# Optimization experiments

Measured on AMD Instinct MI355X. Metric: run time of the kernel, lower is better.

## Reference

```python
import jax, jax.numpy as jnp
import numpy as np

D_MODEL = 1024
NUM_HEADS = 16
HEAD_DIM = D_MODEL // NUM_HEADS  # 64
# NOTE: the torch module passes scale=attention_head_size (NOT 1/sqrt(dh));
# we reproduce that exact math: scores are MULTIPLIED by head_dim.
SCALE = float(HEAD_DIM)

B, S = 2, 2048


def setup_inputs() -> dict:
    key = jax.random.key(0)
    ks = jax.random.split(key, 6)
    q = jax.random.normal(ks[0], (B, S, D_MODEL), dtype=jnp.float32)
    k = jax.random.normal(ks[1], (B, S, D_MODEL), dtype=jnp.float32)
    v = jax.random.normal(ks[2], (B, S, D_MODEL), dtype=jnp.float32)
    # Linear weights stored as [in, out]; scaled like typical init so the
    # (head_dim-scaled) logits stay numerically sane.
    w_std = 0.02
    Wq = jax.random.normal(ks[3], (D_MODEL, D_MODEL), dtype=jnp.float32) * w_std
    Wk = jax.random.normal(ks[4], (D_MODEL, D_MODEL), dtype=jnp.float32) * w_std
    Wv = jax.random.normal(ks[5], (D_MODEL, D_MODEL), dtype=jnp.float32) * w_std
    return {"q": q, "k": k, "v": v, "Wq": Wq, "Wk": Wk, "Wv": Wv}


def reference(q, k, v, Wq, Wk, Wv):
    Bq, Sq, _ = q.shape
    # QKV projections (qkv_bias=False), split into heads: [B, S, H, dh]
    qh = (q @ Wq).reshape(Bq, Sq, NUM_HEADS, HEAD_DIM)
    kh = (k @ Wk).reshape(Bq, Sq, NUM_HEADS, HEAD_DIM)
    vh = (v @ Wv).reshape(Bq, Sq, NUM_HEADS, HEAD_DIM)
    # Full materialized scores [B, H, Sq, Sk] -- the naive MHA pattern.
    sims = jnp.einsum("bqhd,bkhd->bhqk", qh, kh) * SCALE
    attn = jax.nn.softmax(sims, axis=-1)
    # Second matmul, then merge heads back: [B, S, D]
    out = jnp.einsum("bhqk,bkhd->bqhd", attn, vh).reshape(Bq, Sq, D_MODEL)
    return out
```

## Files before the change

kernel.cpp:

```cpp
#include <hip/hip_runtime.h>
#include <cstdint>
#include <cstddef>

typedef unsigned short u16;
typedef __bf16 bf16x8 __attribute__((ext_vector_type(8)));
typedef float f32x4 __attribute__((ext_vector_type(4)));
typedef unsigned int u32x4 __attribute__((ext_vector_type(4)));
typedef unsigned int u32x2 __attribute__((ext_vector_type(2)));
typedef u16 u16x4 __attribute__((ext_vector_type(4)));

typedef __attribute__((address_space(3))) void lds_void;
typedef __attribute__((address_space(1))) void glb_void;

constexpr float CEXP = 92.33248261689366f;

constexpr size_t XSZ = 4096ull * 1024ull;
constexpr size_t WSZ = 1024ull * 1024ull;
constexpr size_t OFF_XQH = 0;
constexpr size_t OFF_XQL = OFF_XQH + XSZ;
constexpr size_t OFF_XKH = OFF_XQL + XSZ;
constexpr size_t OFF_XKL = OFF_XKH + XSZ;
constexpr size_t OFF_XVH = OFF_XKL + XSZ;
constexpr size_t OFF_XVL = OFF_XVH + XSZ;
constexpr size_t OFF_WQH = OFF_XVL + XSZ;
constexpr size_t OFF_WQL = OFF_WQH + WSZ;
constexpr size_t OFF_WKH = OFF_WQL + WSZ;
constexpr size_t OFF_WKL = OFF_WKH + WSZ;
constexpr size_t OFF_WVH = OFF_WKL + WSZ;
constexpr size_t OFF_WVL = OFF_WVH + WSZ;
constexpr size_t OFF_QH  = OFF_WVL + WSZ;
constexpr size_t OFF_QL  = OFF_QH + XSZ;
constexpr size_t OFF_KH  = OFF_QL + XSZ;
constexpr size_t OFF_KL  = OFF_KH + XSZ;
constexpr size_t OFF_VH  = OFF_KL + XSZ;
constexpr size_t OFF_VT  = OFF_VH + XSZ;

__device__ __forceinline__ u16 f2b(float f) {
  unsigned u = __builtin_bit_cast(unsigned, f);
  return (u16)((u + 0x7FFFu + ((u >> 16) & 1u)) >> 16);
}
__device__ __forceinline__ float b2f(u16 h) {
  return __builtin_bit_cast(float, ((unsigned)h) << 16);
}
__device__ __forceinline__ bf16x8 ld8(const u16* p) {
  return __builtin_bit_cast(bf16x8, *(const u32x4*)p);
}
__device__ __forceinline__ unsigned pk2(float a, float b) {
#if __has_builtin(__builtin_amdgcn_cvt_pk_bf16_f32)
  auto v = __builtin_amdgcn_cvt_pk_bf16_f32(a, b);
  return __builtin_bit_cast(unsigned, v);
#else
  return (unsigned)f2b(a) | ((unsigned)f2b(b) << 16);
#endif
}
__device__ __forceinline__ float ex2(float x) {
#if __has_builtin(__builtin_amdgcn_exp2f)
  return __builtin_amdgcn_exp2f(x);
#else
  return exp2f(x);
#endif
}
__device__ __forceinline__ void glds16(const u16* g, u16* l) {
  __builtin_amdgcn_global_load_lds((const glb_void*)g, (lds_void*)l, 16, 0, 0);
}
__device__ __forceinline__ int swz32(int row, int cg) {
  return row * 32 + ((cg ^ ((row >> 1) & 3)) * 8);
}
__device__ __forceinline__ int swz64(int row, int cg) {
  return row * 64 + ((cg ^ (row & 7)) * 8);
}

__global__ __launch_bounds__(256) void convert_all(const float* __restrict__ q,
                                                   const float* __restrict__ k,
                                                   const float* __restrict__ v,
                                                   const float* __restrict__ Wq,
                                                   const float* __restrict__ Wk,
                                                   const float* __restrict__ Wv,
                                                   u16* __restrict__ ws) {
  __shared__ float tile[32][33];
  int id = blockIdx.x;
  int t = threadIdx.x;
  if (id < 12288) {
    int z = id >> 12, blk = id & 4095;
    const float* in = (z == 0) ? q : (z == 1) ? k : v;
    u16* hi = ws + ((z == 0) ? OFF_XQH : (z == 1) ? OFF_XKH : OFF_XVH);
    u16* lo = ws + ((z == 0) ? OFF_XQL : (z == 1) ? OFF_XKL : OFF_XVL);
    size_t i = ((size_t)blk * 256u + t) * 4u;
    float4 vv = *(const float4*)(in + i);
    float a[4] = {vv.x, vv.y, vv.z, vv.w};
    u16x4 hv, lv;
#pragma unroll
    for (int j = 0; j < 4; ++j) {
      u16 hb = f2b(a[j]);
      hv[j] = hb;
      lv[j] = f2b(a[j] - b2f(hb));
    }
    *(u16x4*)(hi + i) = hv;
    if (z != 2) *(u16x4*)(lo + i) = lv;
  } else {
    int r0 = id - 12288;
    int z = r0 >> 10, rem = r0 & 1023;
    const float* W = (z == 0) ? Wq : (z == 1) ? Wk : Wv;
    u16* hiT = ws + ((z == 0) ? OFF_WQH : (z == 1) ? OFF_WKH : OFF_WVH);
    u16* loT = ws + ((z == 0) ? OFF_WQL : (z == 1) ? OFF_WKL : OFF_WVL);
    int n0 = (rem & 31) * 32, k0 = (rem >> 5) * 32;
    int r = t >> 3, c0 = (t & 7) * 4;
    float4 vv = *(const float4*)(W + (size_t)(k0 + r) * 1024 + n0 + c0);
    tile[r][c0] = vv.x; tile[r][c0 + 1] = vv.y; tile[r][c0 + 2] = vv.z; tile[r][c0 + 3] = vv.w;
    __syncthreads();
    u16x4 hv, lv;
#pragma unroll
    for (int j = 0; j < 4; ++j) {
      float x = tile[c0 + j][r];
      u16 hb = f2b(x);
      hv[j] = hb;
      lv[j] = f2b(x - b2f(hb));
    }
    size_t o = (size_t)(n0 + r) * 1024 + k0 + c0;
    *(u16x4*)(hiT + o) = hv;
    if (z != 2) *(u16x4*)(loT + o) = lv;
  }
}

__global__ __launch_bounds__(256, 4) void gemm_qkv(u16* __restrict__ ws) {
  __shared__ u16 sA[2][64 * 32];
  __shared__ u16 sB[2][128 * 32];
  u16* cbuf = &sB[0][0];

  int id = blockIdx.x;
  int xcd = id & 7, seq = id >> 3;
  int pair = (seq >> 3) * 8 + xcd;
  int tile_n = seq & 7;
  int z = pair >> 6;
  int tile_m = pair & 63;

  const u16 *Ah, *Al, *Bh, *Bl; u16 *Oh, *Ol; bool split;
  if (z == 0)      { Ah = ws + OFF_XQH; Al = ws + OFF_XQL; Bh = ws + OFF_WQH; Bl = ws + OFF_WQL; Oh = ws + OFF_QH; Ol = ws + OFF_QL; split = true; }
  else if (z == 1) { Ah = ws + OFF_XKH; Al = ws + OFF_XKL; Bh = ws + OFF_WKH; Bl = ws + OFF_WKL; Oh = ws + OFF_KH; Ol = ws + OFF_KL; split = true; }
  else             { Ah = ws + OFF_XVH; Al = nullptr;      Bh = ws + OFF_WVH; Bl = nullptr;      Oh = ws + OFF_VT; Ol = nullptr;    split = false; }
  float oscale = (z == 0) ? CEXP : 1.0f;
  int m0 = tile_m * 64, n0 = tile_n * 128;
  int t = threadIdx.x, lane = t & 63, wave = t >> 6;
  int quad = lane >> 4, l15 = lane & 15;
  int wm = (wave >> 1) * 32, wn = (wave & 1) * 64;
  int rl = lane >> 2, cgl = lane & 3;
  f32x4 acc[2][4] = {};

  int rowA = wave * 16 + rl;
  size_t gA = (size_t)(m0 + rowA) * 1024 + (cgl ^ ((rowA >> 1) & 3)) * 8;
  int lbA = wave * 512;
  size_t gB[2]; int lbB[2];
#pragma unroll
  for (int i = 0; i < 2; ++i) {
    int rowB = wave * 32 + i * 16 + rl;
    gB[i] = (size_t)(n0 + rowB) * 1024 + (cgl ^ ((rowB >> 1) & 3)) * 8;
    lbB[i] = wave * 1024 + i * 512;
  }

  for (int kb = 0; kb < 32; ++kb) {
    int k0 = kb * 32;
    __syncthreads();
    glds16(Ah + gA + k0, &sA[0][lbA]);
    if (split) glds16(Al + gA + k0, &sA[1][lbA]);
#pragma unroll
    for (int i = 0; i < 2; ++i) {
      glds16(Bh + gB[i] + k0, &sB[0][lbB[i]]);
      if (split) glds16(Bl + gB[i] + k0, &sB[1][lbB[i]]);
    }
    __syncthreads();
    bf16x8 afh[2], afl[2], bfh[4], bfl[4];
#pragma unroll
    for (int mt = 0; mt < 2; ++mt) {
      int ra = wm + mt * 16 + l15;
      afh[mt] = ld8(&sA[0][swz32(ra, quad)]);
      if (split) afl[mt] = ld8(&sA[1][swz32(ra, quad)]);
    }
#pragma unroll
    for (int nt = 0; nt < 4; ++nt) {
      int rb = wn + nt * 16 + l15;
      bfh[nt] = ld8(&sB[0][swz32(rb, quad)]);
      if (split) bfl[nt] = ld8(&sB[1][swz32(rb, quad)]);
    }
#pragma unroll
    for (int mt = 0; mt < 2; ++mt)
#pragma unroll
      for (int nt = 0; nt < 4; ++nt) {
        acc[mt][nt] = __builtin_amdgcn_mfma_f32_16x16x32_bf16(afh[mt], bfh[nt], acc[mt][nt], 0, 0, 0);
        if (split) {
          acc[mt][nt] = __builtin_amdgcn_mfma_f32_16x16x32_bf16(afl[mt], bfh[nt], acc[mt][nt], 0, 0, 0);
          acc[mt][nt] = __builtin_amdgcn_mfma_f32_16x16x32_bf16(afh[mt], bfl[nt], acc[mt][nt], 0, 0, 0);
        }
      }
  }
  auto epi_round = [&](u16* dst, bool lo_round) {
#pragma unroll
    for (int mt = 0; mt < 2; ++mt)
#pragma unroll
      for (int nt = 0; nt < 4; ++nt)
#pragma unroll
        for (int r = 0; r < 4; ++r) {
          int row = wm + mt * 16 + quad * 4 + r;
          int col = wn + nt * 16 + l15;
          float v = acc[mt][nt][r] * oscale;
          u16 hb = f2b(v);
          u16 val = lo_round ? f2b(v - b2f(hb)) : hb;
          cbuf[row * 128 + (((col >> 3) ^ (row & 15)) * 8) + (col & 7)] = val;
        }
    __syncthreads();
    int row = t >> 2, seg = t & 3;
    int gm = m0 + row, bb = gm >> 11, s = gm & 2047;
    int hh = (n0 >> 6) + (seg >> 1), d0 = (seg & 1) * 32;
    u16* gp = dst + ((size_t)(bb * 16 + hh) * 2048 + s) * 64 + d0;
#pragma unroll
    for (int i = 0; i < 4; ++i) {
      int phys = (seg * 4 + i) ^ (row & 15);
      *(u32x4*)(gp + i * 8) = *(const u32x4*)(&cbuf[row * 128 + phys * 8]);
    }
  };
  __syncthreads();
  if (split) {
    epi_round(Oh, false);
    __syncthreads();
    epi_round(Ol, true);
  } else {
#pragma unroll
    for (int mt = 0; mt < 2; ++mt)
#pragma unroll
      for (int nt = 0; nt < 4; ++nt)
#pragma unroll
        for (int r = 0; r < 4; ++r) {
          int row = wm + mt * 16 + quad * 4 + r;
          int col = wn + nt * 16 + l15;
          cbuf[row * 128 + (((col >> 3) ^ (row & 15)) * 8) + (col & 7)] =
              f2b(acc[mt][nt][r]);
        }
    __syncthreads();
    int col = t >> 1, sh = t & 1;
    int hg = (n0 + col) >> 6, d = (n0 + col) & 63;
    int bb = m0 >> 11, s0 = m0 & 2047;
    u16 vals[32];
#pragma unroll
    for (int i = 0; i < 32; ++i) {
      int row = sh * 32 + i;
      vals[i] = cbuf[row * 128 + (((col >> 3) ^ (row & 15)) * 8) + (col & 7)];
    }
    u16* gp = Oh + ((size_t)((bb * 16 + hg) * 64 + d)) * 2048 + s0 + sh * 32;
#pragma unroll
    for (int i = 0; i < 4; ++i)
      *(u32x4*)(gp + i * 8) = *(const u32x4*)(&vals[i * 8]);
  }
}

__global__ __launch_bounds__(256, 4) void attn(const u16* __restrict__ ws,
                                               float* __restrict__ out) {
  __shared__ u16 lkh[64 * 64];
  __shared__ u16 lkl[64 * 64];
  __shared__ u16 lvt[64 * 64];
  __shared__ u16 lp[4][16 * 64];
  const u16* Qh = ws + OFF_QH; const u16* Ql = ws + OFF_QL;
  const u16* Kh = ws + OFF_KH; const u16* Kl = ws + OFF_KL;
  const u16* Vt = ws + OFF_VT;
  int id = blockIdx.x;
  int xcd = id & 7, slot = id >> 3;
  int hh = xcd * 4 + (slot >> 5);
  int q0 = (slot & 31) * 64;
  int b = hh >> 4, h = hh & 15;
  int t = threadIdx.x, lane = t & 63, wave = t >> 6;
  int quad = lane >> 4, l15 = lane & 15;
  size_t hb = (size_t)hh * (2048 * 64);
  bf16x8 onesf;
#pragma unroll
  for (int j = 0; j < 8; ++j) onesf[j] = __builtin_bit_cast(__bf16, (u16)0x3F80);
  int qrow = q0 + wave * 16 + l15;
  bf16x8 qfh[2], qfl[2];
#pragma unroll
  for (int ks = 0; ks < 2; ++ks) {
    size_t qo = hb + (size_t)qrow * 64 + ks * 32 + quad * 8;
    qfh[ks] = ld8(Qh + qo);
    qfl[ks] = ld8(Ql + qo);
  }
  float mi = -1e30f;
  f32x4 lsum = {};
  f32x4 o[4] = {};
  int rl = lane >> 3, cgl = lane & 7;

  size_t aK[2], aV[2]; int lb[2];
#pragma unroll
  for (int i = 0; i < 2; ++i) {
    int row = wave * 16 + i * 8 + rl;
    int cgg = cgl ^ (row & 7);
    aK[i] = hb + (size_t)row * 64 + cgg * 8;
    aV[i] = hb + (size_t)row * 2048 + cgg * 8;
    lb[i] = (wave * 16 + i * 8) * 64;
  }
  int soF[2][4];
#pragma unroll
  for (int ks = 0; ks < 2; ++ks)
#pragma unroll
    for (int nt = 0; nt < 4; ++nt)
      soF[ks][nt] = swz64(nt * 16 + l15, ks * 4 + quad);
  int soP[4];
  {
    int r7 = l15 & 7;
#pragma unroll
    for (int nt = 0; nt < 4; ++nt) {
      int c = nt * 2 + (quad >> 1);
      soP[nt] = l15 * 64 + ((c ^ r7) * 8) + (quad & 1) * 4;
    }
  }
  int soPa[2];
#pragma unroll
  for (int ks = 0; ks < 2; ++ks) soPa[ks] = swz64(l15, ks * 4 + quad);
  u16* lpw = &lp[wave][0];

#pragma unroll
  for (int i = 0; i < 2; ++i) {
    glds16(Kh + aK[i], &lkh[lb[i]]);
    glds16(Kl + aK[i], &lkl[lb[i]]);
    glds16(Vt + aV[i], &lvt[lb[i]]);
  }
  __syncthreads();

  for (int kt = 0; kt < 32; ++kt) {
    u32x4 pk_[2], pl_[2], pv_[2];
    if (kt < 31) {
#pragma unroll
      for (int i = 0; i < 2; ++i) {
        pk_[i] = *(const u32x4*)(Kh + aK[i] + (kt + 1) * 4096);
        pl_[i] = *(const u32x4*)(Kl + aK[i] + (kt + 1) * 4096);
        pv_[i] = *(const u32x4*)(Vt + aV[i] + (kt + 1) * 64);
      }
    }
    f32x4 sc[4] = {};
    __builtin_amdgcn_s_setprio(1);
#pragma unroll
    for (int nt = 0; nt < 4; ++nt) {
#pragma unroll
      for (int ks = 0; ks < 2; ++ks) {
        bf16x8 kh_ = ld8(&lkh[soF[ks][nt]]);
        bf16x8 kl_ = ld8(&lkl[soF[ks][nt]]);
        sc[nt] = __builtin_amdgcn_mfma_f32_16x16x32_bf16(kh_, qfh[ks], sc[nt], 0, 0, 0);
        sc[nt] = __builtin_amdgcn_mfma_f32_16x16x32_bf16(kl_, qfh[ks], sc[nt], 0, 0, 0);
        sc[nt] = __builtin_amdgcn_mfma_f32_16x16x32_bf16(kh_, qfl[ks], sc[nt], 0, 0, 0);
      }
    }
    __builtin_amdgcn_s_setprio(0);
    float t0 = fmaxf(fmaxf(sc[0][0], sc[0][1]), sc[0][2]);
    float t1 = fmaxf(fmaxf(sc[0][3], sc[1][0]), sc[1][1]);
    float t2 = fmaxf(fmaxf(sc[1][2], sc[1][3]), sc[2][0]);
    float t3 = fmaxf(fmaxf(sc[2][1], sc[2][2]), sc[2][3]);
    float t4 = fmaxf(fmaxf(sc[3][0], sc[3][1]), sc[3][2]);
    float mx = fmaxf(fmaxf(fmaxf(t0, t1), fmaxf(t2, t3)), fmaxf(t4, sc[3][3]));
    mx = fmaxf(mx, __shfl_xor(mx, 16));
    mx = fmaxf(mx, __shfl_xor(mx, 32));
    float mi_old = mi;
    float mn = fmaxf(mi, mx);
    unsigned long long grew = __ballot(mx > mi);
    mi = mn;
#pragma unroll
    for (int nt = 0; nt < 4; ++nt) {
      unsigned u01 = pk2(ex2(sc[nt][0] - mn), ex2(sc[nt][1] - mn));
      unsigned u23 = pk2(ex2(sc[nt][2] - mn), ex2(sc[nt][3] - mn));
      *(u32x2*)(&lpw[soP[nt]]) = u32x2{u01, u23};
    }
    if (grew) {
      float alpha_s = ex2(mi_old - mn);
      float av[4];
#pragma unroll
      for (int r = 0; r < 4; ++r) av[r] = __shfl(alpha_s, quad * 4 + r);
#pragma unroll
      for (int r = 0; r < 4; ++r) {
        lsum[r] *= av[r];
        o[0][r] *= av[r]; o[1][r] *= av[r]; o[2][r] *= av[r]; o[3][r] *= av[r];
      }
    }
    asm volatile("s_waitcnt lgkmcnt(0)" ::: "memory");
    bf16x8 pa[2];
#pragma unroll
    for (int ks = 0; ks < 2; ++ks) pa[ks] = ld8(&lpw[soPa[ks]]);
    __builtin_amdgcn_s_setprio(1);
    lsum = __builtin_amdgcn_mfma_f32_16x16x32_bf16(pa[0], onesf, lsum, 0, 0, 0);
    lsum = __builtin_amdgcn_mfma_f32_16x16x32_bf16(pa[1], onesf, lsum, 0, 0, 0);
#pragma unroll
    for (int nt = 0; nt < 4; ++nt)
#pragma unroll
      for (int ks = 0; ks < 2; ++ks) {
        bf16x8 bv = ld8(&lvt[soF[ks][nt]]);
        o[nt] = __builtin_amdgcn_mfma_f32_16x16x32_bf16(pa[ks], bv, o[nt], 0, 0, 0);
      }
    __builtin_amdgcn_s_setprio(0);
    __syncthreads();
    if (kt < 31) {
#pragma unroll
      for (int i = 0; i < 2; ++i) {
        *(u32x4*)(&lkh[lb[i] + lane * 8]) = pk_[i];
        *(u32x4*)(&lkl[lb[i] + lane * 8]) = pl_[i];
        *(u32x4*)(&lvt[lb[i] + lane * 8]) = pv_[i];
      }
    }
    __syncthreads();
  }
  float inv[4];
#pragma unroll
  for (int r = 0; r < 4; ++r) inv[r] = 1.0f / lsum[r];
#pragma unroll
  for (int nt = 0; nt < 4; ++nt)
#pragma unroll
    for (int r = 0; r < 4; ++r) {
      int srow = q0 + wave * 16 + quad * 4 + r;
      int d = nt * 16 + l15;
      out[(size_t)(b * 2048 + srow) * 1024 + h * 64 + d] = o[nt][r] * inv[r];
    }
}

extern "C" void kernel_launch(void* const* d_in, const int* in_sizes, int n_in,
                              void* d_out, int out_size, void* d_ws, size_t ws_size,
                              hipStream_t stream) {
  const float* q  = (const float*)d_in[0];
  const float* k  = (const float*)d_in[1];
  const float* v  = (const float*)d_in[2];
  const float* Wq = (const float*)d_in[3];
  const float* Wk = (const float*)d_in[4];
  const float* Wv = (const float*)d_in[5];
  u16* ws = (u16*)d_ws;
  float* out = (float*)d_out;

  convert_all<<<15360, 256, 0, stream>>>(q, k, v, Wq, Wk, Wv, ws);
  gemm_qkv<<<1536, 256, 0, stream>>>(ws);
  attn<<<1024, 256, 0, stream>>>(ws, out);
}
```

Baseline: 270.7 us.

## Process two 16-row query groups per wave and skip negligible score tiles

Each wave now handles 32 query rows as two groups, so every K/V tile loaded into LDS is reused for twice as many queries. The block count halves and the occupancy hint drops to 2. It also skips the exponentiation and PV MFMAs for a group when the tile's max falls far below the running max, treating those probabilities as zero. This trades extra registers and lower occupancy for fewer global loads and less work, and the skip introduces a small approximation.

```diff
diff --git a/kernel.cpp b/kernel.cpp
--- a/kernel.cpp
+++ b/kernel.cpp
@@ -251,19 +251,19 @@
   }
 }
 
-__global__ __launch_bounds__(256, 4) void attn(const u16* __restrict__ ws,
+__global__ __launch_bounds__(256, 2) void attn(const u16* __restrict__ ws,
                                                float* __restrict__ out) {
   __shared__ u16 lkh[64 * 64];
   __shared__ u16 lkl[64 * 64];
   __shared__ u16 lvt[64 * 64];
-  __shared__ u16 lp[4][16 * 64];
+  __shared__ u16 lp[4][2][16 * 64];
   const u16* Qh = ws + OFF_QH; const u16* Ql = ws + OFF_QL;
   const u16* Kh = ws + OFF_KH; const u16* Kl = ws + OFF_KL;
   const u16* Vt = ws + OFF_VT;
   int id = blockIdx.x;
   int xcd = id & 7, slot = id >> 3;
-  int hh = xcd * 4 + (slot >> 5);
-  int q0 = (slot & 31) * 64;
+  int hh = xcd * 4 + (slot >> 4);
+  int q0 = (slot & 15) * 128;
   int b = hh >> 4, h = hh & 15;
   int t = threadIdx.x, lane = t & 63, wave = t >> 6;
   int quad = lane >> 4, l15 = lane & 15;
@@ -271,17 +271,20 @@
   bf16x8 onesf;
 #pragma unroll
   for (int j = 0; j < 8; ++j) onesf[j] = __builtin_bit_cast(__bf16, (u16)0x3F80);
-  int qrow = q0 + wave * 16 + l15;
-  bf16x8 qfh[2], qfl[2];
-#pragma unroll
-  for (int ks = 0; ks < 2; ++ks) {
-    size_t qo = hb + (size_t)qrow * 64 + ks * 32 + quad * 8;
-    qfh[ks] = ld8(Qh + qo);
-    qfl[ks] = ld8(Ql + qo);
-  }
-  float mi = -1e30f;
-  f32x4 lsum = {};
-  f32x4 o[4] = {};
+  bf16x8 qfh[2][2], qfl[2][2];
+#pragma unroll
+  for (int g = 0; g < 2; ++g) {
+    int qrow = q0 + wave * 32 + g * 16 + l15;
+#pragma unroll
+    for (int ks = 0; ks < 2; ++ks) {
+      size_t qo = hb + (size_t)qrow * 64 + ks * 32 + quad * 8;
+      qfh[g][ks] = ld8(Qh + qo);
+      qfl[g][ks] = ld8(Ql + qo);
+    }
+  }
+  float mi[2] = {-1e30f, -1e30f};
+  f32x4 lsum[2] = {};
+  f32x4 o[2][4] = {};
   int rl = lane >> 3, cgl = lane & 7;
 
   size_t aK[2], aV[2]; int lb[2];
@@ -311,7 +314,7 @@
   int soPa[2];
 #pragma unroll
   for (int ks = 0; ks < 2; ++ks) soPa[ks] = swz64(l15, ks * 4 + quad);
-  u16* lpw = &lp[wave][0];
+  u16* lpw[2] = {&lp[wave][0][0], &lp[wave][1][0]};
 
 #pragma unroll
   for (int i = 0; i < 2; ++i) {
@@ -331,7 +334,7 @@
         pv_[i] = *(const u32x4*)(Vt + aV[i] + (kt + 1) * 64);
       }
     }
-    f32x4 sc[4] = {};
+    f32x4 sc[2][4] = {};
     __builtin_amdgcn_s_setprio(1);
 #pragma unroll
     for (int nt = 0; nt < 4; ++nt) {
@@ -339,56 +342,83 @@
       for (int ks = 0; ks < 2; ++ks) {
         bf16x8 kh_ = ld8(&lkh[soF[ks][nt]]);
         bf16x8 kl_ = ld8(&lkl[soF[ks][nt]]);
-        sc[nt] = __builtin_amdgcn_mfma_f32_16x16x32_bf16(kh_, qfh[ks], sc[nt], 0, 0, 0);
-        sc[nt] = __builtin_amdgcn_mfma_f32_16x16x32_bf16(kl_, qfh[ks], sc[nt], 0, 0, 0);
-        sc[nt] = __builtin_amdgcn_mfma_f32_16x16x32_bf16(kh_, qfl[ks], sc[nt], 0, 0, 0);
+#pragma unroll
+        for (int g = 0; g < 2; ++g) {
+          sc[g][nt] = __builtin_amdgcn_mfma_f32_16x16x32_bf16(kh_, qfh[g][ks], sc[g][nt], 0, 0, 0);
+          sc[g][nt] = __builtin_amdgcn_mfma_f32_16x16x32_bf16(kl_, qfh[g][ks], sc[g][nt], 0, 0, 0);
+          sc[g][nt] = __builtin_amdgcn_mfma_f32_16x16x32_bf16(kh_, qfl[g][ks], sc[g][nt], 0, 0, 0);
+        }
       }
     }
     __builtin_amdgcn_s_setprio(0);
-    float t0 = fmaxf(fmaxf(sc[0][0], sc[0][1]), sc[0][2]);
-    float t1 = fmaxf(fmaxf(sc[0][3], sc[1][0]), sc[1][1]);
-    float t2 = fmaxf(fmaxf(sc[1][2], sc[1][3]), sc[2][0]);
-    float t3 = fmaxf(fmaxf(sc[2][1], sc[2][2]), sc[2][3]);
-    float t4 = fmaxf(fmaxf(sc[3][0], sc[3][1]), sc[3][2]);
-    float mx = fmaxf(fmaxf(fmaxf(t0, t1), fmaxf(t2, t3)), fmaxf(t4, sc[3][3]));
-    mx = fmaxf(mx, __shfl_xor(mx, 16));
-    mx = fmaxf(mx, __shfl_xor(mx, 32));
-    float mi_old = mi;
-    float mn = fmaxf(mi, mx);
-    unsigned long long grew = __ballot(mx > mi);
-    mi = mn;
-#pragma unroll
-    for (int nt = 0; nt < 4; ++nt) {
-      unsigned u01 = pk2(ex2(sc[nt][0] - mn), ex2(sc[nt][1] - mn));
-      unsigned u23 = pk2(ex2(sc[nt][2] - mn), ex2(sc[nt][3] - mn));
-      *(u32x2*)(&lpw[soP[nt]]) = u32x2{u01, u23};
-    }
-    if (grew) {
-      float alpha_s = ex2(mi_old - mn);
-      float av[4];
-#pragma unroll
-      for (int r = 0; r < 4; ++r) av[r] = __shfl(alpha_s, quad * 4 + r);
-#pragma unroll
-      for (int r = 0; r < 4; ++r) {
-        lsum[r] *= av[r];
-        o[0][r] *= av[r]; o[1][r] *= av[r]; o[2][r] *= av[r]; o[3][r] *= av[r];
-      }
-    }
-    asm volatile("s_waitcnt lgkmcnt(0)" ::: "memory");
-    bf16x8 pa[2];
-#pragma unroll
-    for (int ks = 0; ks < 2; ++ks) pa[ks] = ld8(&lpw[soPa[ks]]);
-    __builtin_amdgcn_s_setprio(1);
-    lsum = __builtin_amdgcn_mfma_f32_16x16x32_bf16(pa[0], onesf, lsum, 0, 0, 0);
-    lsum = __builtin_amdgcn_mfma_f32_16x16x32_bf16(pa[1], onesf, lsum, 0, 0, 0);
-#pragma unroll
-    for (int nt = 0; nt < 4; ++nt)
-#pragma unroll
-      for (int ks = 0; ks < 2; ++ks) {
-        bf16x8 bv = ld8(&lvt[soF[ks][nt]]);
-        o[nt] = __builtin_amdgcn_mfma_f32_16x16x32_bf16(pa[ks], bv, o[nt], 0, 0, 0);
-      }
-    __builtin_amdgcn_s_setprio(0);
+    bool live[2], grew[2];
+    float mn[2];
+#pragma unroll
+    for (int g = 0; g < 2; ++g) {
+      float t0 = fmaxf(fmaxf(sc[g][0][0], sc[g][0][1]), sc[g][0][2]);
+      float t1 = fmaxf(fmaxf(sc[g][0][3], sc[g][1][0]), sc[g][1][1]);
+      float t2 = fmaxf(fmaxf(sc[g][1][2], sc[g][1][3]), sc[g][2][0]);
+      float t3 = fmaxf(fmaxf(sc[g][2][1], sc[g][2][2]), sc[g][2][3]);
+      float t4 = fmaxf(fmaxf(sc[g][3][0], sc[g][3][1]), sc[g][3][2]);
+      float mx = fmaxf(fmaxf(fmaxf(t0, t1), fmaxf(t2, t3)), fmaxf(t4, sc[g][3][3]));
+      mx = fmaxf(mx, __shfl_xor(mx, 16));
+      mx = fmaxf(mx, __shfl_xor(mx, 32));
+      float mo = mi[g];
+      live[g] = __ballot(mx > mo - 28.0f) != 0ull;
+      grew[g] = __ballot(mx > mo) != 0ull;
+      mn[g] = fmaxf(mo, mx);
+    }
+#pragma unroll
+    for (int g = 0; g < 2; ++g) {
+      if (live[g]) {
+        float m = mn[g];
+#pragma unroll
+        for (int nt = 0; nt < 4; ++nt) {
+          unsigned u01 = pk2(ex2(sc[g][nt][0] - m), ex2(sc[g][nt][1] - m));
+          unsigned u23 = pk2(ex2(sc[g][nt][2] - m), ex2(sc[g][nt][3] - m));
+          *(u32x2*)(&lpw[g][soP[nt]]) = u32x2{u01, u23};
+        }
+        if (grew[g]) {
+          float alpha_s = ex2(mi[g] - m);
+          float av[4];
+#pragma unroll
+          for (int r = 0; r < 4; ++r) av[r] = __shfl(alpha_s, quad * 4 + r);
+#pragma unroll
+          for (int r = 0; r < 4; ++r) {
+            lsum[g][r] *= av[r];
+            o[g][0][r] *= av[r]; o[g][1][r] *= av[r];
+            o[g][2][r] *= av[r]; o[g][3][r] *= av[r];
+          }
+        }
+        mi[g] = m;
+      }
+    }
+    if (live[0] | live[1]) {
+      asm volatile("s_waitcnt lgkmcnt(0)" ::: "memory");
+      bf16x8 pa[2][2];
+#pragma unroll
+      for (int g = 0; g < 2; ++g)
+        if (live[g]) {
+#pragma unroll
+          for (int ks = 0; ks < 2; ++ks) pa[g][ks] = ld8(&lpw[g][soPa[ks]]);
+        }
+      __builtin_amdgcn_s_setprio(1);
+#pragma unroll
+      for (int g = 0; g < 2; ++g)
+        if (live[g]) {
+          lsum[g] = __builtin_amdgcn_mfma_f32_16x16x32_bf16(pa[g][0], onesf, lsum[g], 0, 0, 0);
+          lsum[g] = __builtin_amdgcn_mfma_f32_16x16x32_bf16(pa[g][1], onesf, lsum[g], 0, 0, 0);
+        }
+#pragma unroll
+      for (int nt = 0; nt < 4; ++nt)
+#pragma unroll
+        for (int ks = 0; ks < 2; ++ks) {
+          bf16x8 bv = ld8(&lvt[soF[ks][nt]]);
+          if (live[0]) o[0][nt] = __builtin_amdgcn_mfma_f32_16x16x32_bf16(pa[0][ks], bv, o[0][nt], 0, 0, 0);
+          if (live[1]) o[1][nt] = __builtin_amdgcn_mfma_f32_16x16x32_bf16(pa[1][ks], bv, o[1][nt], 0, 0, 0);
+        }
+      __builtin_amdgcn_s_setprio(0);
+    }
     __syncthreads();
     if (kt < 31) {
 #pragma unroll
@@ -400,17 +430,20 @@
     }
     __syncthreads();
   }
-  float inv[4];
-#pragma unroll
-  for (int r = 0; r < 4; ++r) inv[r] = 1.0f / lsum[r];
-#pragma unroll
-  for (int nt = 0; nt < 4; ++nt)
-#pragma unroll
-    for (int r = 0; r < 4; ++r) {
-      int srow = q0 + wave * 16 + quad * 4 + r;
-      int d = nt * 16 + l15;
-      out[(size_t)(b * 2048 + srow) * 1024 + h * 64 + d] = o[nt][r] * inv[r];
-    }
+#pragma unroll
+  for (int g = 0; g < 2; ++g) {
+    float inv[4];
+#pragma unroll
+    for (int r = 0; r < 4; ++r) inv[r] = 1.0f / lsum[g][r];
+#pragma unroll
+    for (int nt = 0; nt < 4; ++nt)
+#pragma unroll
+      for (int r = 0; r < 4; ++r) {
+        int srow = q0 + wave * 32 + g * 16 + quad * 4 + r;
+        int d = nt * 16 + l15;
+        out[(size_t)(b * 2048 + srow) * 1024 + h * 64 + d] = o[g][nt][r] * inv[r];
+      }
+  }
 }
 
 extern "C" void kernel_launch(void* const* d_in, const int* in_sizes, int n_in,
@@ -427,5 +460,5 @@
 
   convert_all<<<15360, 256, 0, stream>>>(q, k, v, Wq, Wk, Wv, ws);
   gemm_qkv<<<1536, 256, 0, stream>>>(ws);
-  attn<<<1024, 256, 0, stream>>>(ws, out);
-}
+  attn<<<512, 256, 0, stream>>>(ws, out);
+}
```

Result: no change. 270.3 us (-0.2%).
